# Kernel optimization log

Hardware: AMD Instinct MI355X
Metric: run time of the kernel (lower is better)

The kernel has to match this reference:

```python
import jax, jax.numpy as jnp
import numpy as np

ROPE_THETA = 10000.0


def _apply_rope(x, rot_dim):
    # lucidrains RotaryEmbedding: only first rot_dim channels are rotated,
    # freqs are interleave-repeated, rotate_half works on (d r=2) pairs.
    S = x.shape[-2]
    half = rot_dim // 2
    inv_freq = 1.0 / (ROPE_THETA ** (jnp.arange(0, rot_dim, 2, dtype=jnp.float32) / rot_dim))  # [half]
    pos = jnp.arange(S, dtype=jnp.float32)
    freqs = pos[:, None] * inv_freq[None, :]          # [S, half]
    freqs = jnp.repeat(freqs, 2, axis=-1)             # [S, rot_dim] interleaved
    cos = jnp.cos(freqs).astype(x.dtype)
    sin = jnp.sin(freqs).astype(x.dtype)
    xl, xr = x[..., :rot_dim], x[..., rot_dim:]
    xp = xl.reshape(*xl.shape[:-1], half, 2)
    x1, x2 = xp[..., 0], xp[..., 1]
    rot_half = jnp.stack([-x2, x1], axis=-1).reshape(xl.shape)
    return jnp.concatenate([xl * cos + rot_half * sin, xr], axis=-1)


def setup_inputs() -> dict:
    key = jax.random.key(0)
    ks = jax.random.split(key, 7)
    B, Sa, Se, d_audio, d_score = 4, 4096, 2048, 1024, 1024
    d_h = min(d_audio, d_score)
    return {
        "x_audio": jax.random.normal(ks[0], (B, Sa, d_audio), jnp.float32),
        "x_event": jax.random.normal(ks[1], (B, Se, d_score), jnp.float32),
        "event_padding_mask": jax.random.randint(ks[2], (B, Se), 0, 2) > 0,
        "W_q": jax.random.normal(ks[3], (d_h, d_audio), jnp.float32) * (d_audio ** -0.5),
        "b_q": jax.random.normal(ks[4], (d_h,), jnp.float32) * 0.02,
        "W_k": jax.random.normal(ks[5], (d_h, d_score), jnp.float32) * (d_score ** -0.5),
        "b_k": jax.random.normal(ks[6], (d_h,), jnp.float32) * 0.02,
    }


def reference(x_audio, x_event, event_padding_mask, W_q, b_q, W_k, b_k):
    d_h = W_q.shape[0]
    rot_dim = d_h // 2  # RotaryEmbedding(dim=d_h//2) -> partial rotary over first d_h//2 channels
    Q = jnp.einsum("bsd,hd->bsh", x_audio, W_q) + b_q
    K = jnp.einsum("bed,hd->beh", x_event, W_k) + b_k
    Q = _apply_rope(Q, rot_dim)
    K = _apply_rope(K, rot_dim)
    attn = jnp.einsum("bsh,beh->bse", Q, K)  # [B, S_audio, S_event]
    mask = event_padding_mask[:, None, :]     # [B, 1, S_event]
    attn = jnp.where(mask, attn, jnp.float32(-jnp.inf))
    return attn
```

## Files before the change

### kernel.cpp

```cpp
#include <hip/hip_runtime.h>
#include <hip/hip_bf16.h>
#include <cmath>

#define BATCH 4
#define SA 4096
#define SE 2048
#define DIM 1024
#define ROT 512

#define BM 128
#define BN 128
#define BK 32

#define MASK_SENTINEL (-1.0e30f)

using short8  = __attribute__((ext_vector_type(8))) short;
using floatx4 = __attribute__((ext_vector_type(4))) float;

#define RFREQ 0.0519051171f

__device__ __forceinline__ void gl_lds16(const void* g, void* l) {
    __builtin_amdgcn_global_load_lds(
        (const __attribute__((address_space(1))) unsigned int*)g,
        (__attribute__((address_space(3))) unsigned int*)l, 16, 0, 0);
}

__device__ __forceinline__ short bf16_of(float f) {
    __hip_bfloat16 h = __float2bfloat16(f);
    return *reinterpret_cast<short*>(&h);
}

__global__ __launch_bounds__(256) void probe_mask_kernel(
    const int* __restrict__ mask_i, int* __restrict__ flag)
{
    __shared__ int s_bad;
    if (threadIdx.x == 0) s_bad = 0;
    __syncthreads();
    int bad = 0;
    for (int i = threadIdx.x; i < 1024; i += 256) {
        int v = mask_i[i];
        bad |= (v != 0 && v != 1) ? 1 : 0;
    }
    if (bad) atomicOr(&s_bad, 1);
    __syncthreads();
    if (threadIdx.x == 0) *flag = s_bad ? 0 : 1;
}

__global__ __launch_bounds__(256) void cvt_bf16_kernel(
    const float* __restrict__ in, short* __restrict__ out, int n8)
{
    int i = blockIdx.x * 256 + threadIdx.x;
    if (i >= n8) return;
    const float4 f0 = ((const float4*)in)[2 * i];
    const float4 f1 = ((const float4*)in)[2 * i + 1];
    short8 o;
    o[0] = bf16_of(f0.x); o[1] = bf16_of(f0.y);
    o[2] = bf16_of(f0.z); o[3] = bf16_of(f0.w);
    o[4] = bf16_of(f1.x); o[5] = bf16_of(f1.y);
    o[6] = bf16_of(f1.z); o[7] = bf16_of(f1.w);
    ((short8*)out)[i] = o;
}

template <int MODE>
__global__ __launch_bounds__(256) void gemm_bf16_kernel(
    const short* __restrict__ A,
    const short* __restrict__ B,
    const float* __restrict__ bias,
    const void*  __restrict__ maskp,
    const int*   __restrict__ flag,
    void* __restrict__ outp,
    int smask)
{
    __shared__ short lA[BM * BK];
    __shared__ short lB[BN * BK];

    const int tid  = threadIdx.x;
    const int wid  = tid >> 6;
    const int lane = tid & 63;
    const int m0 = blockIdx.y * BM;
    const int n0 = blockIdx.x * BN;
    const int z  = blockIdx.z;

    const short* Ab = A;
    const short* Bb = B;
    if (MODE == 1) {
        Ab += (size_t)z * SA * DIM;
        Bb += (size_t)z * SE * DIM;
    }

    const int srow = lane >> 2;
    const int scol = (lane & 3) * 16;

    const char* gA0 = (const char*)Ab + (size_t)(m0 + 0 * 64 + wid * 16 + srow) * (DIM * 2) + scol;
    const char* gA1 = (const char*)Ab + (size_t)(m0 + 1 * 64 + wid * 16 + srow) * (DIM * 2) + scol;
    const char* gB0 = (const char*)Bb + (size_t)(n0 + 0 * 64 + wid * 16 + srow) * (DIM * 2) + scol;
    const char* gB1 = (const char*)Bb + (size_t)(n0 + 1 * 64 + wid * 16 + srow) * (DIM * 2) + scol;
    char* lA0 = (char*)lA + (0 * 64 + wid * 16 + srow) * 64 + scol;
    char* lA1 = (char*)lA + (1 * 64 + wid * 16 + srow) * 64 + scol;
    char* lB0 = (char*)lB + (0 * 64 + wid * 16 + srow) * 64 + scol;
    char* lB1 = (char*)lB + (1 * 64 + wid * 16 + srow) * 64 + scol;

    const int wm = (wid >> 1) * 64;
    const int wn = (wid & 1) * 64;
    const int fr = lane & 15;
    const int fk = (lane >> 4) * 8;

    int aoff[4], boff[4];
#pragma unroll
    for (int i = 0; i < 4; ++i) {
        aoff[i] = (wm + i * 16 + fr) * BK + fk;
        boff[i] = (wn + i * 16 + fr) * BK + fk;
    }

    floatx4 acc[4][4] = {};

    for (int k0 = 0; k0 < DIM; k0 += BK) {
        const size_t kb = (size_t)k0 * 2;
        __syncthreads();
        gl_lds16(gA0 + kb, lA0);
        gl_lds16(gA1 + kb, lA1);
        gl_lds16(gB0 + kb, lB0);
        gl_lds16(gB1 + kb, lB1);
        __syncthreads();

        short8 af[4], bf[4];
#pragma unroll
        for (int i = 0; i < 4; ++i) af[i] = *(const short8*)&lA[aoff[i]];
#pragma unroll
        for (int i = 0; i < 4; ++i) bf[i] = *(const short8*)&lB[boff[i]];
#pragma unroll
        for (int mi = 0; mi < 4; ++mi)
#pragma unroll
            for (int ni = 0; ni < 4; ++ni)
                acc[mi][ni] = __builtin_amdgcn_mfma_f32_16x16x32_bf16(
                    af[mi], bf[ni], acc[mi][ni], 0, 0, 0);
    }

    const int rrow = (lane >> 4) * 4;

    if (MODE == 0) {
        short* out = (short*)outp;
#pragma unroll
        for (int ni = 0; ni < 4; ++ni) {
            const int h = n0 + wn + ni * 16 + fr;
            const float bv  = bias[h];
            const bool rope = (h < ROT);
            const float inv = rope ? exp2f(-RFREQ * (float)(h >> 1)) : 0.f;
            const float sgn = (h & 1) ? 1.f : -1.f;
#pragma unroll
            for (int mi = 0; mi < 4; ++mi) {
                const int rbase = m0 + wm + mi * 16 + rrow;
#pragma unroll
                for (int r = 0; r < 4; ++r) {
                    float v = acc[mi][ni][r] + bv;
                    float p = __shfl_xor(v, 1);
                    if (rope) {
                        const float ang = (float)((rbase + r) & smask) * inv;
                        float s, c;
                        sincosf(ang, &s, &c);
                        v = v * c + sgn * p * s;
                    }
                    out[(size_t)(rbase + r) * DIM + h] = bf16_of(v);
                }
            }
        }
    } else {
        float* out = (float*)outp + (size_t)z * SA * SE;
        const int fl = *flag;
#pragma unroll
        for (int ni = 0; ni < 4; ++ni) {
            const int e = n0 + wn + ni * 16 + fr;
            int mk;
            if (fl) mk = ((const int*)maskp)[(size_t)z * SE + e];
            else    mk = ((const unsigned char*)maskp)[(size_t)z * SE + e];
#pragma unroll
            for (int mi = 0; mi < 4; ++mi) {
                const int rbase = m0 + wm + mi * 16 + rrow;
#pragma unroll
                for (int r = 0; r < 4; ++r) {
                    const float v = mk ? acc[mi][ni][r] : MASK_SENTINEL;
                    out[(size_t)(rbase + r) * SE + e] = v;
                }
            }
        }
    }
}

extern "C" void kernel_launch(void* const* d_in, const int* in_sizes, int n_in,
                              void* d_out, int out_size, void* d_ws, size_t ws_size,
                              hipStream_t stream)
{
    const float* x_audio = (const float*)d_in[0];
    const float* x_event = (const float*)d_in[1];
    const void*  maskp   = d_in[2];
    const float* W_q     = (const float*)d_in[3];
    const float* b_q     = (const float*)d_in[4];
    const float* W_k     = (const float*)d_in[5];
    const float* b_k     = (const float*)d_in[6];
    float* out = (float*)d_out;

    char* ws = (char*)d_ws;
    short* xbf  = (short*)(ws);
    short* Qbf  = (short*)(ws + (size_t)32 * 1024 * 1024);
    short* Kbf  = (short*)(ws + (size_t)64 * 1024 * 1024);
    short* Wqbf = (short*)(ws + (size_t)80 * 1024 * 1024);
    short* Wkbf = (short*)(ws + (size_t)82 * 1024 * 1024);
    int*   flag = (int*)  (ws + (size_t)84 * 1024 * 1024);

    probe_mask_kernel<<<1, 256, 0, stream>>>((const int*)maskp, flag);

    const int nxa8 = BATCH * SA * DIM / 8;
    const int nxe8 = BATCH * SE * DIM / 8;
    const int nw8  = DIM * DIM / 8;

    cvt_bf16_kernel<<<(nxa8 + 255) / 256, 256, 0, stream>>>(x_audio, xbf, nxa8);
    cvt_bf16_kernel<<<(nw8 + 255) / 256, 256, 0, stream>>>(W_q, Wqbf, nw8);
    gemm_bf16_kernel<0><<<dim3(DIM / BN, (BATCH * SA) / BM, 1), 256, 0, stream>>>(
        xbf, Wqbf, b_q, nullptr, nullptr, Qbf, SA - 1);

    cvt_bf16_kernel<<<(nxe8 + 255) / 256, 256, 0, stream>>>(x_event, xbf, nxe8);
    cvt_bf16_kernel<<<(nw8 + 255) / 256, 256, 0, stream>>>(W_k, Wkbf, nw8);
    gemm_bf16_kernel<0><<<dim3(DIM / BN, (BATCH * SE) / BM, 1), 256, 0, stream>>>(
        xbf, Wkbf, b_k, nullptr, nullptr, Kbf, SE - 1);

    gemm_bf16_kernel<1><<<dim3(SE / BN, SA / BM, BATCH), 256, 0, stream>>>(
        Qbf, Kbf, nullptr, maskp, flag, out, 0);
}
```

Baseline: 430.9 us.

## Precompute RoPE cos/sin table and swizzle block order for L2 locality

Adds a kernel that builds a cos/sin table for all 256 frequency pairs and 4096 positions, stored in the output buffer as scratch. The projection epilogue then reads this table instead of calling sincosf per element. Block indices are also remapped with an 8-way XCD-style swizzle so that neighbouring tiles share L2 on MI355X. The cost is an extra 8 MB table write and epilogue table reads, plus reliance on the output buffer being overwritten later by the attention GEMM.

```diff
diff --git a/kernel.cpp b/kernel.cpp
--- a/kernel.cpp
+++ b/kernel.cpp
@@ -61,11 +61,23 @@
     ((short8*)out)[i] = o;
 }
 
+__global__ __launch_bounds__(256) void rope_table_kernel(float2* __restrict__ tab)
+{
+    const int i   = blockIdx.x * 256 + threadIdx.x;
+    const int h2  = i >> 12;
+    const int pos = i & 4095;
+    const float inv = exp2f(-RFREQ * (float)h2);
+    float s, c;
+    sincosf((float)pos * inv, &s, &c);
+    tab[i] = make_float2(c, s);
+}
+
 template <int MODE>
-__global__ __launch_bounds__(256) void gemm_bf16_kernel(
+__device__ __forceinline__ void gemm_body(
     const short* __restrict__ A,
     const short* __restrict__ B,
     const float* __restrict__ bias,
+    const float2* __restrict__ ct,
     const void*  __restrict__ maskp,
     const int*   __restrict__ flag,
     void* __restrict__ outp,
@@ -77,15 +89,24 @@
     const int tid  = threadIdx.x;
     const int wid  = tid >> 6;
     const int lane = tid & 63;
-    const int m0 = blockIdx.y * BM;
-    const int n0 = blockIdx.x * BN;
-    const int z  = blockIdx.z;
+
+    const int nbx = gridDim.x, nby = gridDim.y;
+    const int id  = blockIdx.x + nbx * (blockIdx.y + nby * blockIdx.z);
+    const int cpx = (nbx * nby * gridDim.z) >> 3;
+    const int swz = (id & 7) * cpx + (id >> 3);
+    const int bx  = swz % nbx;
+    const int byz = swz / nbx;
+    const int by  = byz % nby;
+    const int bz  = byz / nby;
+
+    const int m0 = by * BM;
+    const int n0 = bx * BN;
 
     const short* Ab = A;
     const short* Bb = B;
     if (MODE == 1) {
-        Ab += (size_t)z * SA * DIM;
-        Bb += (size_t)z * SE * DIM;
+        Ab += (size_t)bz * SA * DIM;
+        Bb += (size_t)bz * SE * DIM;
     }
 
     const int srow = lane >> 2;
@@ -145,34 +166,35 @@
             const int h = n0 + wn + ni * 16 + fr;
             const float bv  = bias[h];
             const bool rope = (h < ROT);
-            const float inv = rope ? exp2f(-RFREQ * (float)(h >> 1)) : 0.f;
             const float sgn = (h & 1) ? 1.f : -1.f;
+            const float2* ctrow = ct + ((size_t)(h >> 1) << 12);
 #pragma unroll
             for (int mi = 0; mi < 4; ++mi) {
                 const int rbase = m0 + wm + mi * 16 + rrow;
+                const int pbase = rbase & smask;
+                float2 cs[4];
+                if (rope) {
+#pragma unroll
+                    for (int r = 0; r < 4; ++r) cs[r] = ctrow[pbase + r];
+                }
 #pragma unroll
                 for (int r = 0; r < 4; ++r) {
                     float v = acc[mi][ni][r] + bv;
                     float p = __shfl_xor(v, 1);
-                    if (rope) {
-                        const float ang = (float)((rbase + r) & smask) * inv;
-                        float s, c;
-                        sincosf(ang, &s, &c);
-                        v = v * c + sgn * p * s;
-                    }
+                    if (rope) v = v * cs[r].x + sgn * p * cs[r].y;
                     out[(size_t)(rbase + r) * DIM + h] = bf16_of(v);
                 }
             }
         }
     } else {
-        float* out = (float*)outp + (size_t)z * SA * SE;
+        float* out = (float*)outp + (size_t)bz * SA * SE;
         const int fl = *flag;
 #pragma unroll
         for (int ni = 0; ni < 4; ++ni) {
             const int e = n0 + wn + ni * 16 + fr;
             int mk;
-            if (fl) mk = ((const int*)maskp)[(size_t)z * SE + e];
-            else    mk = ((const unsigned char*)maskp)[(size_t)z * SE + e];
+            if (fl) mk = ((const int*)maskp)[(size_t)bz * SE + e];
+            else    mk = ((const unsigned char*)maskp)[(size_t)bz * SE + e];
 #pragma unroll
             for (int mi = 0; mi < 4; ++mi) {
                 const int rbase = m0 + wm + mi * 16 + rrow;
@@ -184,6 +206,22 @@
             }
         }
     }
+}
+
+__global__ __launch_bounds__(256) void gemm_proj_kernel(
+    const short* __restrict__ A, const short* __restrict__ B,
+    const float* __restrict__ bias, const float2* __restrict__ ct,
+    short* __restrict__ out, int smask)
+{
+    gemm_body<0>(A, B, bias, ct, nullptr, nullptr, out, smask);
+}
+
+__global__ __launch_bounds__(256) void gemm_attn_kernel(
+    const short* __restrict__ Q, const short* __restrict__ K,
+    const void* __restrict__ maskp, const int* __restrict__ flag,
+    float* __restrict__ out)
+{
+    gemm_body<1>(Q, K, nullptr, nullptr, maskp, flag, out, 0);
 }
 
 extern "C" void kernel_launch(void* const* d_in, const int* in_sizes, int n_in,
@@ -206,8 +244,10 @@
     short* Wqbf = (short*)(ws + (size_t)80 * 1024 * 1024);
     short* Wkbf = (short*)(ws + (size_t)82 * 1024 * 1024);
     int*   flag = (int*)  (ws + (size_t)84 * 1024 * 1024);
+    float2* ct  = (float2*)d_out;
 
     probe_mask_kernel<<<1, 256, 0, stream>>>((const int*)maskp, flag);
+    rope_table_kernel<<<4096, 256, 0, stream>>>(ct);
 
     const int nxa8 = BATCH * SA * DIM / 8;
     const int nxe8 = BATCH * SE * DIM / 8;
@@ -215,14 +255,14 @@
 
     cvt_bf16_kernel<<<(nxa8 + 255) / 256, 256, 0, stream>>>(x_audio, xbf, nxa8);
     cvt_bf16_kernel<<<(nw8 + 255) / 256, 256, 0, stream>>>(W_q, Wqbf, nw8);
-    gemm_bf16_kernel<0><<<dim3(DIM / BN, (BATCH * SA) / BM, 1), 256, 0, stream>>>(
-        xbf, Wqbf, b_q, nullptr, nullptr, Qbf, SA - 1);
+    gemm_proj_kernel<<<dim3(DIM / BN, (BATCH * SA) / BM, 1), 256, 0, stream>>>(
+        xbf, Wqbf, b_q, ct, Qbf, SA - 1);
 
     cvt_bf16_kernel<<<(nxe8 + 255) / 256, 256, 0, stream>>>(x_event, xbf, nxe8);
     cvt_bf16_kernel<<<(nw8 + 255) / 256, 256, 0, stream>>>(W_k, Wkbf, nw8);
-    gemm_bf16_kernel<0><<<dim3(DIM / BN, (BATCH * SE) / BM, 1), 256, 0, stream>>>(
-        xbf, Wkbf, b_k, nullptr, nullptr, Kbf, SE - 1);
-
-    gemm_bf16_kernel<1><<<dim3(SE / BN, SA / BM, BATCH), 256, 0, stream>>>(
-        Qbf, Kbf, nullptr, maskp, flag, out, 0);
-}
+    gemm_proj_kernel<<<dim3(DIM / BN, (BATCH * SE) / BM, 1), 256, 0, stream>>>(
+        xbf, Wkbf, b_k, ct, Kbf, SE - 1);
+
+    gemm_attn_kernel<<<dim3(SE / BN, SA / BM, BATCH), 256, 0, stream>>>(
+        Qbf, Kbf, maskp, flag, out);
+}
```

New measurement: 408.8 us. 1.05x faster.
